# Performance work log

Hardware: AMD Instinct MI355X
Metric: run time of the kernel (lower is better)

Reference implementation:

```python
import jax, jax.numpy as jnp
import numpy as np

N = 30000   # fluid particles
E = 480000  # edges
F = 4       # fluidFeatures (in channels)
P = 8       # RBF basis size per dim (dims=[8], 1D)
LAYERS = [32, 64, 64, 2]


def hat_basis(x, n):
    # 'linear' RBF: hat functions on n evenly spaced centers in [-1, 1]
    centers = jnp.linspace(-1.0, 1.0, n, dtype=x.dtype)
    spacing = 2.0 / (n - 1)
    return jnp.maximum(0.0, 1.0 - jnp.abs(x[:, None] - centers[None, :]) / spacing)  # [E, n]


def rbf_conv(x, fi, fj, d, W, b, mask, n_nodes):
    # x: [N, Cin]; d: [E, 1] clamped; W: [P, Cin, Cout]; b: [Cout]
    phi = hat_basis(d[:, 0], W.shape[0])      # [E, P]
    xj = x[fj]                                 # gather source features [E, Cin]
    msg = jnp.zeros((xj.shape[0], W.shape[2]), dtype=x.dtype)
    for p in range(W.shape[0]):                # small fixed P=8 loop keeps memory O(E*Cout)
        msg = msg + phi[:, p, None] * (xj @ W[p])
    msg = jnp.where(mask[:, None], msg, 0.0)   # centerIgnore: drop self edges fi==fj
    out = jax.ops.segment_sum(msg, fi, num_segments=n_nodes)  # scatter-reduce to targets
    return out + b


def _xavier(key, shape_in, shape_out):
    lim = float(np.sqrt(6.0 / (shape_in + shape_out)))
    return jax.random.uniform(key, (shape_in, shape_out), jnp.float32, -lim, lim)


def setup_inputs() -> dict:
    key = jax.random.key(0)
    ks = jax.random.split(key, 16)
    fluidFeatures = jax.random.normal(ks[0], (N, F), jnp.float32)
    fi = jax.random.randint(ks[1], (E,), 0, N)
    fj = jax.random.randint(ks[2], (E,), 0, N)
    distances = jax.random.normal(ks[3], (E, 1), jnp.float32)
    # conv channels: 4->32, 64->64, 64->64, 64->2
    cio = [(F, 32), (2 * 32, 64), (64, 64), (64, 2)]
    inp = {"fluidFeatures": fluidFeatures, "fi": fi, "fj": fj, "distances": distances}
    for li, (ci, co) in enumerate(cio):
        inp[f"cW{li}"] = jax.random.normal(ks[4 + li], (P, ci, co), jnp.float32) * (1.0 / np.sqrt(P * ci))
        inp[f"cb{li}"] = jnp.zeros((co,), jnp.float32)
        inp[f"fW{li}"] = _xavier(ks[8 + li], ci, co)   # stored [in, out]
        inp[f"fb{li}"] = jnp.zeros((co,), jnp.float32)
    return inp


def reference(fluidFeatures, fi, fj, distances,
              cW0, cb0, fW0, fb0, cW1, cb1, fW1, fb1,
              cW2, cb2, fW2, fb2, cW3, cb3, fW3, fb3):
    n_nodes = fluidFeatures.shape[0]
    mask = fi != fj                     # centerIgnore (mask instead of filter: jit-safe)
    d = jnp.clip(distances, -1.0, 1.0)

    conv0 = rbf_conv(fluidFeatures, fi, fj, d, cW0, cb0, mask, n_nodes)  # [N, 32]
    lin0 = fluidFeatures @ fW0 + fb0                                      # [N, 32]
    ans = jnp.concatenate([lin0, conv0], axis=1)                          # [N, 64]

    # i = 1: features[0]=32 != features[1]=64 -> no residual
    ansc = jax.nn.relu(ans)
    ans = rbf_conv(ansc, fi, fj, d, cW1, cb1, mask, n_nodes) + (ansc @ fW1 + fb1)
    # i = 2: features[1]==features[2]==64 and shapes match -> residual
    ansc = jax.nn.relu(ans)
    ans = rbf_conv(ansc, fi, fj, d, cW2, cb2, mask, n_nodes) + (ansc @ fW2 + fb2) + ans
    # i = 3: 64 -> 2, no residual
    ansc = jax.nn.relu(ans)
    ans = rbf_conv(ansc, fi, fj, d, cW3, cb3, mask, n_nodes) + (ansc @ fW3 + fb3)

    return ans  # dim == 1 (dims=[8]) -> no /128
```

## Files before the change

### kernel.cpp

```cpp
#include <hip/hip_runtime.h>


#define CAP 48

typedef __attribute__((ext_vector_type(8))) short short8;
typedef __attribute__((ext_vector_type(4))) short short4v;
typedef __attribute__((ext_vector_type(4))) float f32x4;

__device__ __forceinline__ short bf16s(float f) {
  unsigned u = __float_as_uint(f);
  return (short)((u + 0x7FFF + ((u >> 16) & 1)) >> 16);
}
__device__ __forceinline__ float b2f(unsigned short s) {
  return __uint_as_float(((unsigned)s) << 16);
}
__device__ __forceinline__ unsigned pack2(float a, float b) {
  return (unsigned)(unsigned short)bf16s(a) | ((unsigned)(unsigned short)bf16s(b) << 16);
}
__device__ __forceinline__ float dec_w0(int v) {
  return __uint_as_float(0x3F800000u | (((unsigned)v & 0xFFFu) << 11)) - 1.0f;
}
__device__ __forceinline__ float dec_sf(int v) {
  return (float)(((unsigned)v >> 12) & 1u);
}

__global__ void fill_prep(const float* __restrict__ dist,
                          const int* __restrict__ fi, const int* __restrict__ fj,
                          int* __restrict__ cnt, int* __restrict__ jw, int nE,
                          const float* __restrict__ cW1, const float* __restrict__ fW1,
                          const float* __restrict__ cW2, const float* __restrict__ fW2,
                          short* __restrict__ wt1, short* __restrict__ wt2,
                          const float* __restrict__ X,
                          const float* __restrict__ cW0,
                          const float* __restrict__ fW0,
                          unsigned short* __restrict__ U0, int n,
                          int fillBlocks, int prepBlocks) {
  if ((int)blockIdx.x < fillBlocks) {
    int e = blockIdx.x * blockDim.x + threadIdx.x;
    if (e >= nE) return;
    int i = fi[e], j = fj[e];
    if (i == j) return;
    float d = fminf(1.0f, fmaxf(-1.0f, dist[e]));
    float u = (d + 1.0f) * 3.5f;
    int p = min((int)u, 6);
    float w0 = 1.0f - (u - (float)p);
    int wq = min((int)(w0 * 4096.0f + 0.5f), 4095);
    unsigned off = (unsigned)(j * 9 + p);
    int pos = atomicAdd(&cnt[i], 1);
    if (pos < CAP)
      jw[(size_t)i * CAP + pos] = (int)((off << 13) | 0x1000u | (unsigned)wq);
  } else if ((int)blockIdx.x < fillBlocks + prepBlocks) {
    int idx = ((int)blockIdx.x - fillBlocks) * blockDim.x + threadIdx.x;
    if (idx >= 2 * 576 * 64) return;
    int sel = idx / (576 * 64);
    int r = idx - sel * (576 * 64);
    int col = r >> 6, ch = r & 63;
    const float* cW = sel ? cW2 : cW1;
    const float* fW = sel ? fW2 : fW1;
    float v;
    if (col < 512) {
      int p = col >> 6, co = col & 63;
      v = cW[((size_t)p * 64 + ch) * 64 + co];
    } else {
      v = fW[(size_t)ch * 64 + (col - 512)];
    }
    (sel ? wt2 : wt1)[(size_t)col * 64 + ch] = bf16s(v);
  } else {
    int idx = ((int)blockIdx.x - fillBlocks - prepBlocks) * blockDim.x + threadIdx.x;
    if (idx >= n * 72) return;
    int i = idx / 72, g = idx - i * 72;
    float4 x = *(const float4*)(X + (size_t)i * 4);
    float xk[4] = {x.x, x.y, x.z, x.w};
    float s[4] = {0, 0, 0, 0};
    if (g < 64) {
      int p = g >> 3;
      int co = (g * 4) & 31;
      #pragma unroll
      for (int k = 0; k < 4; ++k) {
        const float* wr = cW0 + ((size_t)p * 4 + k) * 32 + co;
        #pragma unroll
        for (int c = 0; c < 4; ++c) s[c] = fmaf(xk[k], wr[c], s[c]);
      }
    } else {
      int co = (g - 64) * 4;
      #pragma unroll
      for (int k = 0; k < 4; ++k) {
        const float* wr = fW0 + (size_t)k * 32 + co;
        #pragma unroll
        for (int c = 0; c < 4; ++c) s[c] = fmaf(xk[k], wr[c], s[c]);
      }
    }
    uint2 pk = make_uint2(pack2(s[0], s[1]), pack2(s[2], s[3]));
    *(uint2*)(U0 + (size_t)i * 288 + g * 4) = pk;
  }
}

__device__ __forceinline__ void gemm_tail(const unsigned short* sXa, short* sUL,
                                          const short* __restrict__ WT,
                                          int w, int lane) {
  const int mrow = lane & 15;
  const int quad = lane >> 4;
  short8 b0 = *(const short8*)(sXa + mrow * 64 + quad * 8);
  short8 b1 = *(const short8*)(sXa + mrow * 64 + quad * 8 + 32);
  const short* A0 = WT + (size_t)(w * 16 + mrow) * 64 + quad * 8;
  const short* A1 = WT + (size_t)((w + 16) * 16 + mrow) * 64 + quad * 8;
  short8 a00 = *(const short8*)(A0);
  short8 a01 = *(const short8*)(A0 + 32);
  short8 a10 = *(const short8*)(A1);
  short8 a11 = *(const short8*)(A1 + 32);
  const bool has3 = (w < 4);
  short8 a20 = {0, 0, 0, 0, 0, 0, 0, 0};
  short8 a21 = {0, 0, 0, 0, 0, 0, 0, 0};
  if (has3) {
    const short* A2 = WT + (size_t)((w + 32) * 16 + mrow) * 64 + quad * 8;
    a20 = *(const short8*)(A2);
    a21 = *(const short8*)(A2 + 32);
  }
  __builtin_amdgcn_sched_barrier(0);
  f32x4 acc0 = {0, 0, 0, 0}, acc1 = {0, 0, 0, 0};
  acc0 = __builtin_amdgcn_mfma_f32_16x16x32_bf16(a00, b0, acc0, 0, 0, 0);
  acc0 = __builtin_amdgcn_mfma_f32_16x16x32_bf16(a01, b1, acc0, 0, 0, 0);
  acc1 = __builtin_amdgcn_mfma_f32_16x16x32_bf16(a10, b0, acc1, 0, 0, 0);
  acc1 = __builtin_amdgcn_mfma_f32_16x16x32_bf16(a11, b1, acc1, 0, 0, 0);
  short4v pk;
  #pragma unroll
  for (int r = 0; r < 4; ++r) pk[r] = bf16s(acc0[r]);
  *(short4v*)(sUL + mrow * 584 + w * 16 + quad * 4) = pk;
  #pragma unroll
  for (int r = 0; r < 4; ++r) pk[r] = bf16s(acc1[r]);
  *(short4v*)(sUL + mrow * 584 + (w + 16) * 16 + quad * 4) = pk;
  if (has3) {
    f32x4 acc2 = {0, 0, 0, 0};
    acc2 = __builtin_amdgcn_mfma_f32_16x16x32_bf16(a20, b0, acc2, 0, 0, 0);
    acc2 = __builtin_amdgcn_mfma_f32_16x16x32_bf16(a21, b1, acc2, 0, 0, 0);
    #pragma unroll
    for (int r = 0; r < 4; ++r) pk[r] = bf16s(acc2[r]);
    *(short4v*)(sUL + mrow * 584 + (w + 32) * 16 + quad * 4) = pk;
  }
}

__global__ __launch_bounds__(1024, 8) void layer0_gemm(
    const unsigned short* __restrict__ U0,
    const int* __restrict__ cnt, const int* __restrict__ jw,
    const float* __restrict__ cb0, const float* __restrict__ fb0,
    const short* __restrict__ WTul,
    unsigned short* __restrict__ UL, int n) {
  __shared__ __align__(16) unsigned short sXa[16 * 64];
  __shared__ __align__(16) short sUL[16 * 584];
  const int tid = threadIdx.x;
  const int w = tid >> 6;
  const int lane = tid & 63;
  const int grp = lane >> 5;
  const int gl = lane & 31;
  const unsigned gl4 = (unsigned)gl * 4u;
  const int nodeBase = blockIdx.x * 16;
  const int i = nodeBase + w;
  const bool valid = (i < n);
  const int ic = valid ? i : 0;
  const char* __restrict__ u0B = (const char*)U0;

  int rec = jw[(size_t)ic * CAP + (lane < CAP ? lane : 0)];
  const int m = valid ? min(cnt[ic], CAP) : 0;
  float accLo = 0.0f, accHi = 0.0f;
  unsigned rA[8], rB[8];
  float wA[8], wB[8];
#define L0_LOAD(R, WS, Q0)                                                  \
  _Pragma("unroll")                                                         \
  for (int k = 0; k < 8; ++k) {                                             \
    int vA = __builtin_amdgcn_readlane(rec, (Q0) + 2 * k);                  \
    int vB = __builtin_amdgcn_readlane(rec, (Q0) + 2 * k + 1);              \
    int v = grp ? vB : vA;                                                  \
    unsigned voff = (((unsigned)v >> 7) & 0xFFFFFFC0u) + gl4;               \
    R[k] = *(const unsigned*)(u0B + voff);                                  \
    float w0 = dec_w0(v);                                                   \
    WS[k] = (gl < 16) ? w0 : (dec_sf(v) - w0);                              \
  }
#define L0_FMA(R, WS)                                                       \
  _Pragma("unroll")                                                         \
  for (int k = 0; k < 8; ++k) {                                             \
    accLo = fmaf(WS[k], __uint_as_float(R[k] << 16), accLo);                \
    accHi = fmaf(WS[k], __uint_as_float(R[k] & 0xFFFF0000u), accHi);        \
  }
  if (m > 0) {
    L0_LOAD(rA, wA, 0);
    L0_LOAD(rB, wB, 16);
    __builtin_amdgcn_sched_barrier(0);
    L0_FMA(rA, wA);
    if (m > 16) {
      L0_FMA(rB, wB);
      for (int q0 = 32; q0 < m; q0 += 16) {
        L0_LOAD(rA, wA, q0);
        __builtin_amdgcn_sched_barrier(0);
        L0_FMA(rA, wA);
      }
    }
  }
#undef L0_LOAD
#undef L0_FMA
  accLo += __shfl_xor(accLo, 16, 64);
  accHi += __shfl_xor(accHi, 16, 64);
  accLo += __shfl_xor(accLo, 32, 64);
  accHi += __shfl_xor(accHi, 32, 64);
  if (lane < 16) {
    const int l = lane;
    float c0v = fmaxf(accLo + cb0[2 * l], 0.0f);
    float c1v = fmaxf(accHi + cb0[2 * l + 1], 0.0f);
    unsigned lr = ((const unsigned*)(U0 + (size_t)ic * 288 + 256))[l];
    float l0 = fmaxf(__uint_as_float(lr << 16) + fb0[2 * l], 0.0f);
    float l1 = fmaxf(__uint_as_float(lr & 0xFFFF0000u) + fb0[2 * l + 1], 0.0f);
    unsigned* row = (unsigned*)(sXa + w * 64);
    row[l] = pack2(l0, l1);
    row[16 + l] = pack2(c0v, c1v);
  }
  __syncthreads();

  gemm_tail(sXa, sUL, WTul, w, lane);
  __syncthreads();
  const int r = tid >> 6;
  const int c0 = tid & 63;
  if (nodeBase + r < n) {
    unsigned short* dst = UL + (size_t)(nodeBase + r) * 576;
    #pragma unroll
    for (int chunk = c0; chunk < 72; chunk += 64)
      *(short8*)(dst + chunk * 8) = *(const short8*)(sUL + r * 584 + chunk * 8);
  }
}

__global__ __launch_bounds__(1024, 8) void conv_gemm(
    const unsigned short* __restrict__ ULA,
    const int* __restrict__ cnt, const int* __restrict__ jw,
    const float* __restrict__ cb, const float* __restrict__ fb,
    const short* __restrict__ WTul2,
    float* __restrict__ outAns,
    unsigned short* __restrict__ ULB, int n) {
  __shared__ __align__(16) unsigned short sXa[16 * 64];
  __shared__ __align__(16) short sUL[16 * 584];
  const int tid = threadIdx.x;
  const int w = tid >> 6;
  const int lane = tid & 63;
  const int half = lane >> 5;
  const int pl = lane & 31;
  const unsigned lane4 = (unsigned)lane * 4u;
  const int nodeBase = blockIdx.x * 16;
  const int i = nodeBase + w;
  const bool valid = (i < n);
  const int ic = valid ? i : 0;
  const char* __restrict__ ulB = (const char*)ULA;

  int rec = jw[(size_t)ic * CAP + (lane < CAP ? lane : 0)];
  const int m = valid ? min(cnt[ic], CAP) : 0;
  const unsigned Lraw = ((const unsigned*)(ULA + (size_t)ic * 576 + 512))[pl];
  float accLo = 0.0f, accHi = 0.0f;
  unsigned rA[16], rB[16];
#define C1_LOAD(R, Q0)                                                     \
  _Pragma("unroll")                                                        \
  for (int k = 0; k < 16; ++k) {                                           \
    int v = __builtin_amdgcn_readlane(rec, (Q0) + k);                      \
    unsigned voff = (((unsigned)v >> 6) & 0xFFFFFF80u) + lane4;            \
    R[k] = *(const unsigned*)(ulB + voff);                                 \
  }
#define C1_FMA(R, Q0)                                                      \
  _Pragma("unroll")                                                        \
  for (int k = 0; k < 16; ++k) {                                           \
    int v = __builtin_amdgcn_readlane(rec, (Q0) + k);                      \
    float w0 = dec_w0(v);                                                  \
    float wv = half ? (dec_sf(v) - w0) : w0;                               \
    accLo = fmaf(wv, __uint_as_float(R[k] << 16), accLo);                  \
    accHi = fmaf(wv, __uint_as_float(R[k] & 0xFFFF0000u), accHi);          \
  }
  if (m > 0) {
    C1_LOAD(rA, 0);
    C1_LOAD(rB, 16);
    __builtin_amdgcn_sched_barrier(0);
    C1_FMA(rA, 0);
    if (m > 16) {
      C1_FMA(rB, 16);
      for (int q0 = 32; q0 < m; q0 += 16) {
        C1_LOAD(rA, q0);
        __builtin_amdgcn_sched_barrier(0);
        C1_FMA(rA, q0);
      }
    }
  }
#undef C1_LOAD
#undef C1_FMA
  accLo += __shfl_xor(accLo, 32, 64);
  accHi += __shfl_xor(accHi, 32, 64);
  if (half == 0) {
    unsigned* row = (unsigned*)(sXa + w * 64);
    if (valid) {
      const int c0i = 2 * pl, c1i = c0i + 1;
      float o0 = accLo + __uint_as_float(Lraw << 16) + cb[c0i] + fb[c0i];
      float o1 = accHi + __uint_as_float(Lraw & 0xFFFF0000u) + cb[c1i] + fb[c1i];
      *(float2*)(outAns + (size_t)i * 64 + c0i) = make_float2(o0, o1);
      row[pl] = pack2(fmaxf(o0, 0.0f), fmaxf(o1, 0.0f));
    } else {
      row[pl] = 0u;
    }
  }
  __syncthreads();

  gemm_tail(sXa, sUL, WTul2, w, lane);
  __syncthreads();
  const int r = tid >> 6;
  const int c0 = tid & 63;
  if (nodeBase + r < n) {
    unsigned short* dst = ULB + (size_t)(nodeBase + r) * 576;
    #pragma unroll
    for (int chunk = c0; chunk < 72; chunk += 64)
      *(short8*)(dst + chunk * 8) = *(const short8*)(sUL + r * 584 + chunk * 8);
  }
}

__global__ __launch_bounds__(256, 8) void conv2_kernel(
    const unsigned short* __restrict__ UL,
    const int* __restrict__ cnt, const int* __restrict__ jw,
    const float* __restrict__ cb, const float* __restrict__ fb,
    const float* __restrict__ resid,
    const float* __restrict__ cW3,
    float* __restrict__ T,
    unsigned short* __restrict__ outAnsc, int n) {
  const int lane = threadIdx.x & 63;
  const int half = lane >> 5;
  const int pl = lane & 31;
  const unsigned lane4 = (unsigned)lane * 4u;
  const int i = (blockIdx.x * blockDim.x + threadIdx.x) >> 6;
  if (i >= n) return;
  const char* __restrict__ ulB = (const char*)UL;
  int rec = jw[(size_t)i * CAP + (lane < CAP ? lane : 0)];
  const int m = min(cnt[i], CAP);
  const unsigned Lraw = ((const unsigned*)(UL + (size_t)i * 576 + 512))[pl];
  float2 rv = *(const float2*)(resid + (size_t)i * 64 + 2 * pl);
  float accLo = 0.0f, accHi = 0.0f;
  unsigned rA[16], rB[16];
#define C2_LOAD(R, Q0)                                                     \
  _Pragma("unroll")                                                        \
  for (int k = 0; k < 16; ++k) {                                           \
    int v = __builtin_amdgcn_readlane(rec, (Q0) + k);                      \
    unsigned voff = (((unsigned)v >> 6) & 0xFFFFFF80u) + lane4;            \
    R[k] = *(const unsigned*)(ulB + voff);                                 \
  }
#define C2_FMA(R, Q0)                                                      \
  _Pragma("unroll")                                                        \
  for (int k = 0; k < 16; ++k) {                                           \
    int v = __builtin_amdgcn_readlane(rec, (Q0) + k);                      \
    float w0 = dec_w0(v);                                                  \
    float wv = half ? (dec_sf(v) - w0) : w0;                               \
    accLo = fmaf(wv, __uint_as_float(R[k] << 16), accLo);                  \
    accHi = fmaf(wv, __uint_as_float(R[k] & 0xFFFF0000u), accHi);          \
  }
  if (m > 0) {
    C2_LOAD(rA, 0);
    C2_LOAD(rB, 16);
    __builtin_amdgcn_sched_barrier(0);
    C2_FMA(rA, 0);
    if (m > 16) {
      C2_FMA(rB, 16);
      for (int q0 = 32; q0 < m; q0 += 16) {
        C2_LOAD(rA, q0);
        __builtin_amdgcn_sched_barrier(0);
        C2_FMA(rA, q0);
      }
    }
  }
#undef C2_LOAD
#undef C2_FMA
  accLo += __shfl_xor(accLo, 32, 64);
  accHi += __shfl_xor(accHi, 32, 64);
  if (half == 0) {
    const int c0i = 2 * pl, c1i = c0i + 1;
    float o0 = accLo + __uint_as_float(Lraw << 16) + cb[c0i] + fb[c0i] + rv.x;
    float o1 = accHi + __uint_as_float(Lraw & 0xFFFF0000u) + cb[c1i] + fb[c1i] + rv.y;
    unsigned short xb0 = (unsigned short)bf16s(fmaxf(o0, 0.0f));
    unsigned short xb1 = (unsigned short)bf16s(fmaxf(o1, 0.0f));
    ((unsigned*)(outAnsc + (size_t)i * 64))[pl] = (unsigned)xb0 | ((unsigned)xb1 << 16);
    float x0 = b2f(xb0), x1 = b2f(xb1);
    float c[16];
    #pragma unroll
    for (int t = 0; t < 16; ++t) {
      const float* wrow = cW3 + ((size_t)(t >> 1) * 64) * 2 + (t & 1);
      c[t] = x0 * wrow[c0i * 2] + x1 * wrow[c1i * 2];
    }
    #pragma unroll
    for (int off = 16; off > 0; off >>= 1) {
      #pragma unroll
      for (int t = 0; t < 16; ++t) c[t] += __shfl_xor(c[t], off, 64);
    }
    if (pl == 0) {
      float* tr = T + (size_t)i * 18;
      #pragma unroll
      for (int t = 0; t < 16; ++t) tr[t] = c[t];
    }
  }
}

__global__ __launch_bounds__(256, 4) void layer3_kernel(
    const unsigned short* __restrict__ Xb,
    const float* __restrict__ T,
    const int* __restrict__ cnt, const int* __restrict__ jw,
    const float* __restrict__ cb3, const float* __restrict__ fb3,
    const float* __restrict__ fW3,
    float* __restrict__ out, int n) {
  const int lane = threadIdx.x & 63;
  const int i = (blockIdx.x * blockDim.x + threadIdx.x) >> 6;
  if (i >= n) return;
  const int m = min(cnt[i], CAP);
  float c0 = 0.0f, c1 = 0.0f;
  if (lane < m) {
    int v = jw[(size_t)i * CAP + lane];
    unsigned off = (unsigned)v >> 13;
    float w0 = dec_w0(v);
    float w1 = 1.0f - w0;
    const float* tb = T + (size_t)off * 2;
    float2 ta = *(const float2*)(tb);
    float2 tc = *(const float2*)(tb + 2);
    c0 = w0 * ta.x + w1 * tc.x;
    c1 = w0 * ta.y + w1 * tc.y;
  }
  float xi = b2f(Xb[(size_t)i * 64 + lane]);
  float2 fw = *(const float2*)(fW3 + lane * 2);
  c0 = fmaf(xi, fw.x, c0);
  c1 = fmaf(xi, fw.y, c1);
  #pragma unroll
  for (int off = 32; off > 0; off >>= 1) {
    c0 += __shfl_xor(c0, off, 64);
    c1 += __shfl_xor(c1, off, 64);
  }
  if (lane == 0) {
    out[(size_t)i * 2 + 0] = c0 + cb3[0] + fb3[0];
    out[(size_t)i * 2 + 1] = c1 + cb3[1] + fb3[1];
  }
}

extern "C" void kernel_launch(void* const* d_in, const int* in_sizes, int n_in,
                              void* d_out, int out_size, void* d_ws, size_t ws_size,
                              hipStream_t stream) {
  const float* X    = (const float*)d_in[0];
  const int*   fi   = (const int*)d_in[1];
  const int*   fj   = (const int*)d_in[2];
  const float* dist = (const float*)d_in[3];
  const float* cW0 = (const float*)d_in[4];  const float* cb0 = (const float*)d_in[5];
  const float* fW0 = (const float*)d_in[6];  const float* fb0 = (const float*)d_in[7];
  const float* cW1 = (const float*)d_in[8];  const float* cb1 = (const float*)d_in[9];
  const float* fW1 = (const float*)d_in[10]; const float* fb1 = (const float*)d_in[11];
  const float* cW2 = (const float*)d_in[12]; const float* cb2 = (const float*)d_in[13];
  const float* fW2 = (const float*)d_in[14]; const float* fb2 = (const float*)d_in[15];
  const float* cW3 = (const float*)d_in[16]; const float* cb3 = (const float*)d_in[17];
  const float* fW3 = (const float*)d_in[18]; const float* fb3 = (const float*)d_in[19];
  float* out = (float*)d_out;

  const int n  = in_sizes[0] / 4;
  const int nE = in_sizes[1];

  unsigned short* ULA   = (unsigned short*)d_ws;
  unsigned short* ULB   = ULA + (size_t)n * 576;
  unsigned short* U0    = ULB;
  float*          ans1  = (float*)(ULB + (size_t)n * 576);
  unsigned short* ansc2 = (unsigned short*)(ans1 + (size_t)n * 64);
  float* T     = (float*)(ansc2 + (size_t)n * 64);
  short* wtul1 = (short*)(T + (size_t)n * 18);
  short* wtul2 = wtul1 + 576 * 64;
  int*   jw    = (int*)(wtul2 + 576 * 64);
  int*   cnt   = jw + (size_t)n * CAP;

  hipMemsetAsync(jw, 0, ((size_t)n * CAP + n) * sizeof(int), stream);
  const int fillBlocks = (nE + 255) / 256;
  const int prepBlocks = (2 * 576 * 64 + 255) / 256;
  const int u0Blocks   = (n * 72 + 255) / 256;
  fill_prep<<<fillBlocks + prepBlocks + u0Blocks, 256, 0, stream>>>(
      dist, fi, fj, cnt, jw, nE, cW1, fW1, cW2, fW2, wtul1, wtul2,
      X, cW0, fW0, U0, n, fillBlocks, prepBlocks);

  layer0_gemm<<<(n + 15) / 16, 1024, 0, stream>>>(U0, cnt, jw, cb0, fb0,
                                                  wtul1, ULA, n);
  conv_gemm<<<(n + 15) / 16, 1024, 0, stream>>>(ULA, cnt, jw, cb1, fb1,
                                                wtul2, ans1, ULB, n);
  conv2_kernel<<<(n * 64 + 255) / 256, 256, 0, stream>>>(
      ULB, cnt, jw, cb2, fb2, ans1, cW3, T, ansc2, n);
  layer3_kernel<<<(n * 64 + 255) / 256, 256, 0, stream>>>(ansc2, T, cnt, jw,
                                                          cb3, fb3, fW3, out, n);
}
```

Before: 244.0 us.

## Load neighbor records via scalar loads and gather with inline-asm SGPR-based loads

Neighbor record rows and counts now come in through scalar s_load_dwordx4 instructions into SGPRs, replacing per-lane vector loads followed by readlane. The gathers use inline-asm global_load_dword with an SGPR base and VGPR offsets, issuing 16 or 32 loads before a single wait. The aim is to cut VALU and readlane overhead and raise memory-level parallelism in the gather loops. In exchange it adds heavy SGPR use, full vmcnt(0) waits with no overlap between batches, and inline asm that depends on the scalar-load alignment of rows.

```diff
diff --git a/kernel.cpp b/kernel.cpp
--- a/kernel.cpp
+++ b/kernel.cpp
@@ -6,6 +6,7 @@
 typedef __attribute__((ext_vector_type(8))) short short8;
 typedef __attribute__((ext_vector_type(4))) short short4v;
 typedef __attribute__((ext_vector_type(4))) float f32x4;
+typedef int v4i __attribute__((ext_vector_type(4)));
 
 __device__ __forceinline__ short bf16s(float f) {
   unsigned u = __float_as_uint(f);
@@ -23,6 +24,96 @@
 __device__ __forceinline__ float dec_sf(int v) {
   return (float)(((unsigned)v >> 12) & 1u);
 }
+__device__ __forceinline__ unsigned long long rfl64(unsigned long long x) {
+  unsigned lo = __builtin_amdgcn_readfirstlane((unsigned)x);
+  unsigned hi = __builtin_amdgcn_readfirstlane((unsigned)(x >> 32));
+  return ((unsigned long long)hi << 32) | (unsigned long long)lo;
+}
+
+#define LOAD_RECS32(JROW, CPTR, RC, MRAW)                                   \
+  {                                                                         \
+    v4i s0_, s1_, s2_, s3_, s4_, s5_, s6_, s7_;                             \
+    asm volatile(                                                           \
+        "s_load_dwordx4 %0, %9, 0x0\n\t"                                    \
+        "s_load_dwordx4 %1, %9, 0x10\n\t"                                   \
+        "s_load_dwordx4 %2, %9, 0x20\n\t"                                   \
+        "s_load_dwordx4 %3, %9, 0x30\n\t"                                   \
+        "s_load_dwordx4 %4, %9, 0x40\n\t"                                   \
+        "s_load_dwordx4 %5, %9, 0x50\n\t"                                   \
+        "s_load_dwordx4 %6, %9, 0x60\n\t"                                   \
+        "s_load_dwordx4 %7, %9, 0x70\n\t"                                   \
+        "s_load_dword %8, %10, 0x0\n\t"                                     \
+        "s_waitcnt lgkmcnt(0)"                                              \
+        : "=&s"(s0_), "=&s"(s1_), "=&s"(s2_), "=&s"(s3_),                   \
+          "=&s"(s4_), "=&s"(s5_), "=&s"(s6_), "=&s"(s7_), "=&s"(MRAW)       \
+        : "s"(JROW), "s"(CPTR)                                              \
+        : "memory");                                                        \
+    _Pragma("unroll") for (int z_ = 0; z_ < 4; ++z_) {                      \
+      RC[z_] = s0_[z_];      RC[4 + z_] = s1_[z_];                          \
+      RC[8 + z_] = s2_[z_];  RC[12 + z_] = s3_[z_];                         \
+      RC[16 + z_] = s4_[z_]; RC[20 + z_] = s5_[z_];                         \
+      RC[24 + z_] = s6_[z_]; RC[28 + z_] = s7_[z_];                         \
+    }                                                                       \
+  }
+
+#define LOAD_RECS16T(JROW, RT)                                              \
+  {                                                                         \
+    v4i t0_, t1_, t2_, t3_;                                                 \
+    asm volatile(                                                           \
+        "s_load_dwordx4 %0, %4, 0x80\n\t"                                   \
+        "s_load_dwordx4 %1, %4, 0x90\n\t"                                   \
+        "s_load_dwordx4 %2, %4, 0xA0\n\t"                                   \
+        "s_load_dwordx4 %3, %4, 0xB0\n\t"                                   \
+        "s_waitcnt lgkmcnt(0)"                                              \
+        : "=&s"(t0_), "=&s"(t1_), "=&s"(t2_), "=&s"(t3_)                    \
+        : "s"(JROW)                                                         \
+        : "memory");                                                        \
+    _Pragma("unroll") for (int z_ = 0; z_ < 4; ++z_) {                      \
+      RT[z_] = t0_[z_];      RT[4 + z_] = t1_[z_];                          \
+      RT[8 + z_] = t2_[z_];  RT[12 + z_] = t3_[z_];                         \
+    }                                                                       \
+  }
+
+#define GLDI(x) "global_load_dword %" #x ", %" #x ", %[bb]\n\t"
+
+#define GATHER8(R, BASE)                                                    \
+  asm volatile(                                                             \
+      GLDI(0) GLDI(1) GLDI(2) GLDI(3) GLDI(4) GLDI(5) GLDI(6) GLDI(7)       \
+      "s_waitcnt vmcnt(0)"                                                  \
+      : "+v"(R[0]), "+v"(R[1]), "+v"(R[2]), "+v"(R[3]), "+v"(R[4]),         \
+        "+v"(R[5]), "+v"(R[6]), "+v"(R[7])                                  \
+      : [bb] "s"(BASE)                                                      \
+      : "memory")
+
+#define GATHER16(R, BASE)                                                   \
+  asm volatile(                                                             \
+      GLDI(0) GLDI(1) GLDI(2) GLDI(3) GLDI(4) GLDI(5) GLDI(6) GLDI(7)       \
+      GLDI(8) GLDI(9) GLDI(10) GLDI(11) GLDI(12) GLDI(13) GLDI(14) GLDI(15) \
+      "s_waitcnt vmcnt(0)"                                                  \
+      : "+v"(R[0]), "+v"(R[1]), "+v"(R[2]), "+v"(R[3]), "+v"(R[4]),         \
+        "+v"(R[5]), "+v"(R[6]), "+v"(R[7]), "+v"(R[8]), "+v"(R[9]),         \
+        "+v"(R[10]), "+v"(R[11]), "+v"(R[12]), "+v"(R[13]), "+v"(R[14]),    \
+        "+v"(R[15])                                                         \
+      : [bb] "s"(BASE)                                                      \
+      : "memory")
+
+#define GATHER32(R, BASE)                                                   \
+  asm volatile(                                                             \
+      GLDI(0) GLDI(1) GLDI(2) GLDI(3) GLDI(4) GLDI(5) GLDI(6) GLDI(7)       \
+      GLDI(8) GLDI(9) GLDI(10) GLDI(11) GLDI(12) GLDI(13) GLDI(14) GLDI(15) \
+      GLDI(16) GLDI(17) GLDI(18) GLDI(19) GLDI(20) GLDI(21) GLDI(22)        \
+      GLDI(23) GLDI(24) GLDI(25) GLDI(26) GLDI(27) GLDI(28) GLDI(29)        \
+      GLDI(30) GLDI(31)                                                     \
+      "s_waitcnt vmcnt(0)"                                                  \
+      : "+v"(R[0]), "+v"(R[1]), "+v"(R[2]), "+v"(R[3]), "+v"(R[4]),         \
+        "+v"(R[5]), "+v"(R[6]), "+v"(R[7]), "+v"(R[8]), "+v"(R[9]),         \
+        "+v"(R[10]), "+v"(R[11]), "+v"(R[12]), "+v"(R[13]), "+v"(R[14]),    \
+        "+v"(R[15]), "+v"(R[16]), "+v"(R[17]), "+v"(R[18]), "+v"(R[19]),    \
+        "+v"(R[20]), "+v"(R[21]), "+v"(R[22]), "+v"(R[23]), "+v"(R[24]),    \
+        "+v"(R[25]), "+v"(R[26]), "+v"(R[27]), "+v"(R[28]), "+v"(R[29]),    \
+        "+v"(R[30]), "+v"(R[31])                                            \
+      : [bb] "s"(BASE)                                                      \
+      : "memory")
 
 __global__ void fill_prep(const float* __restrict__ dist,
                           const int* __restrict__ fi, const int* __restrict__ fj,
@@ -157,46 +248,56 @@
   const int i = nodeBase + w;
   const bool valid = (i < n);
   const int ic = valid ? i : 0;
-  const char* __restrict__ u0B = (const char*)U0;
-
-  int rec = jw[(size_t)ic * CAP + (lane < CAP ? lane : 0)];
-  const int m = valid ? min(cnt[ic], CAP) : 0;
+  const int* jrow = (const int*)rfl64((unsigned long long)(jw + (size_t)ic * CAP));
+  const int* cptr = (const int*)rfl64((unsigned long long)(cnt + ic));
+
+  int rc[32]; int mraw;
+  LOAD_RECS32(jrow, cptr, rc, mraw);
+  const int m = valid ? min(mraw, CAP) : 0;
   float accLo = 0.0f, accHi = 0.0f;
-  unsigned rA[8], rB[8];
-  float wA[8], wB[8];
-#define L0_LOAD(R, WS, Q0)                                                  \
-  _Pragma("unroll")                                                         \
-  for (int k = 0; k < 8; ++k) {                                             \
-    int vA = __builtin_amdgcn_readlane(rec, (Q0) + 2 * k);                  \
-    int vB = __builtin_amdgcn_readlane(rec, (Q0) + 2 * k + 1);              \
-    int v = grp ? vB : vA;                                                  \
-    unsigned voff = (((unsigned)v >> 7) & 0xFFFFFFC0u) + gl4;               \
-    R[k] = *(const unsigned*)(u0B + voff);                                  \
-    float w0 = dec_w0(v);                                                   \
-    WS[k] = (gl < 16) ? w0 : (dec_sf(v) - w0);                              \
-  }
-#define L0_FMA(R, WS)                                                       \
-  _Pragma("unroll")                                                         \
-  for (int k = 0; k < 8; ++k) {                                             \
-    accLo = fmaf(WS[k], __uint_as_float(R[k] << 16), accLo);                \
-    accHi = fmaf(WS[k], __uint_as_float(R[k] & 0xFFFF0000u), accHi);        \
+  unsigned r[16];
+  int vsel[16];
+#define L0_FMA1(K)                                                          \
+  {                                                                         \
+    float w0_ = dec_w0(vsel[K]);                                            \
+    float wgt_ = (gl < 16) ? w0_ : (dec_sf(vsel[K]) - w0_);                 \
+    accLo = fmaf(wgt_, __uint_as_float(r[K] << 16), accLo);                 \
+    accHi = fmaf(wgt_, __uint_as_float(r[K] & 0xFFFF0000u), accHi);         \
   }
   if (m > 0) {
-    L0_LOAD(rA, wA, 0);
-    L0_LOAD(rB, wB, 16);
-    __builtin_amdgcn_sched_barrier(0);
-    L0_FMA(rA, wA);
-    if (m > 16) {
-      L0_FMA(rB, wB);
-      for (int q0 = 32; q0 < m; q0 += 16) {
-        L0_LOAD(rA, wA, q0);
-        __builtin_amdgcn_sched_barrier(0);
-        L0_FMA(rA, wA);
-      }
-    }
-  }
-#undef L0_LOAD
-#undef L0_FMA
+    if (m <= 16) {
+      #pragma unroll
+      for (int k = 0; k < 8; ++k) {
+        vsel[k] = grp ? rc[2 * k + 1] : rc[2 * k];
+        r[k] = ((((unsigned)vsel[k]) >> 7) & 0xFFFFFFC0u) + gl4;
+      }
+      GATHER8(r, U0);
+      #pragma unroll
+      for (int k = 0; k < 8; ++k) L0_FMA1(k);
+    } else {
+      #pragma unroll
+      for (int k = 0; k < 16; ++k) {
+        vsel[k] = grp ? rc[2 * k + 1] : rc[2 * k];
+        r[k] = ((((unsigned)vsel[k]) >> 7) & 0xFFFFFFC0u) + gl4;
+      }
+      GATHER16(r, U0);
+      #pragma unroll
+      for (int k = 0; k < 16; ++k) L0_FMA1(k);
+      if (m > 32) {
+        int rt[16];
+        LOAD_RECS16T(jrow, rt);
+        #pragma unroll
+        for (int k = 0; k < 8; ++k) {
+          vsel[k] = grp ? rt[2 * k + 1] : rt[2 * k];
+          r[k] = ((((unsigned)vsel[k]) >> 7) & 0xFFFFFFC0u) + gl4;
+        }
+        GATHER8(r, U0);
+        #pragma unroll
+        for (int k = 0; k < 8; ++k) L0_FMA1(k);
+      }
+    }
+  }
+#undef L0_FMA1
   accLo += __shfl_xor(accLo, 16, 64);
   accHi += __shfl_xor(accHi, 16, 64);
   accLo += __shfl_xor(accLo, 32, 64);
@@ -216,13 +317,13 @@
 
   gemm_tail(sXa, sUL, WTul, w, lane);
   __syncthreads();
-  const int r = tid >> 6;
+  const int r2 = tid >> 6;
   const int c0 = tid & 63;
-  if (nodeBase + r < n) {
-    unsigned short* dst = UL + (size_t)(nodeBase + r) * 576;
+  if (nodeBase + r2 < n) {
+    unsigned short* dst = UL + (size_t)(nodeBase + r2) * 576;
     #pragma unroll
     for (int chunk = c0; chunk < 72; chunk += 64)
-      *(short8*)(dst + chunk * 8) = *(const short8*)(sUL + r * 584 + chunk * 8);
+      *(short8*)(dst + chunk * 8) = *(const short8*)(sUL + r2 * 584 + chunk * 8);
   }
 }
 
@@ -245,45 +346,47 @@
   const int i = nodeBase + w;
   const bool valid = (i < n);
   const int ic = valid ? i : 0;
-  const char* __restrict__ ulB = (const char*)ULA;
-
-  int rec = jw[(size_t)ic * CAP + (lane < CAP ? lane : 0)];
-  const int m = valid ? min(cnt[ic], CAP) : 0;
+  const int* jrow = (const int*)rfl64((unsigned long long)(jw + (size_t)ic * CAP));
+  const int* cptr = (const int*)rfl64((unsigned long long)(cnt + ic));
+
+  int rc[32]; int mraw;
+  LOAD_RECS32(jrow, cptr, rc, mraw);
+  const int m = valid ? min(mraw, CAP) : 0;
   const unsigned Lraw = ((const unsigned*)(ULA + (size_t)ic * 576 + 512))[pl];
   float accLo = 0.0f, accHi = 0.0f;
-  unsigned rA[16], rB[16];
-#define C1_LOAD(R, Q0)                                                     \
-  _Pragma("unroll")                                                        \
-  for (int k = 0; k < 16; ++k) {                                           \
-    int v = __builtin_amdgcn_readlane(rec, (Q0) + k);                      \
-    unsigned voff = (((unsigned)v >> 6) & 0xFFFFFF80u) + lane4;            \
-    R[k] = *(const unsigned*)(ulB + voff);                                 \
-  }
-#define C1_FMA(R, Q0)                                                      \
-  _Pragma("unroll")                                                        \
-  for (int k = 0; k < 16; ++k) {                                           \
-    int v = __builtin_amdgcn_readlane(rec, (Q0) + k);                      \
-    float w0 = dec_w0(v);                                                  \
-    float wv = half ? (dec_sf(v) - w0) : w0;                               \
-    accLo = fmaf(wv, __uint_as_float(R[k] << 16), accLo);                  \
-    accHi = fmaf(wv, __uint_as_float(R[k] & 0xFFFF0000u), accHi);          \
+  unsigned r[32];
+#define CV_OFF(V) (((((unsigned)(V)) >> 6) & 0xFFFFFF80u) + lane4)
+#define CV_FMA(V, RD)                                                       \
+  {                                                                         \
+    float w0_ = dec_w0(V);                                                  \
+    float wv_ = half ? (dec_sf(V) - w0_) : w0_;                             \
+    accLo = fmaf(wv_, __uint_as_float((RD) << 16), accLo);                  \
+    accHi = fmaf(wv_, __uint_as_float((RD) & 0xFFFF0000u), accHi);          \
   }
   if (m > 0) {
-    C1_LOAD(rA, 0);
-    C1_LOAD(rB, 16);
-    __builtin_amdgcn_sched_barrier(0);
-    C1_FMA(rA, 0);
-    if (m > 16) {
-      C1_FMA(rB, 16);
-      for (int q0 = 32; q0 < m; q0 += 16) {
-        C1_LOAD(rA, q0);
-        __builtin_amdgcn_sched_barrier(0);
-        C1_FMA(rA, q0);
-      }
-    }
-  }
-#undef C1_LOAD
-#undef C1_FMA
+    if (m <= 16) {
+      #pragma unroll
+      for (int k = 0; k < 16; ++k) r[k] = CV_OFF(rc[k]);
+      GATHER16(r, ULA);
+      #pragma unroll
+      for (int k = 0; k < 16; ++k) CV_FMA(rc[k], r[k]);
+    } else {
+      #pragma unroll
+      for (int k = 0; k < 32; ++k) r[k] = CV_OFF(rc[k]);
+      GATHER32(r, ULA);
+      #pragma unroll
+      for (int k = 0; k < 32; ++k) CV_FMA(rc[k], r[k]);
+      if (m > 32) {
+        int rt[16];
+        LOAD_RECS16T(jrow, rt);
+        #pragma unroll
+        for (int k = 0; k < 16; ++k) r[k] = CV_OFF(rt[k]);
+        GATHER16(r, ULA);
+        #pragma unroll
+        for (int k = 0; k < 16; ++k) CV_FMA(rt[k], r[k]);
+      }
+    }
+  }
   accLo += __shfl_xor(accLo, 32, 64);
   accHi += __shfl_xor(accHi, 32, 64);
   if (half == 0) {
@@ -302,13 +405,13 @@
 
   gemm_tail(sXa, sUL, WTul2, w, lane);
   __syncthreads();
-  const int r = tid >> 6;
+  const int r2 = tid >> 6;
   const int c0 = tid & 63;
-  if (nodeBase + r < n) {
-    unsigned short* dst = ULB + (size_t)(nodeBase + r) * 576;
+  if (nodeBase + r2 < n) {
+    unsigned short* dst = ULB + (size_t)(nodeBase + r2) * 576;
     #pragma unroll
     for (int chunk = c0; chunk < 72; chunk += 64)
-      *(short8*)(dst + chunk * 8) = *(const short8*)(sUL + r * 584 + chunk * 8);
+      *(short8*)(dst + chunk * 8) = *(const short8*)(sUL + r2 * 584 + chunk * 8);
   }
 }
 
@@ -326,45 +429,39 @@
   const unsigned lane4 = (unsigned)lane * 4u;
   const int i = (blockIdx.x * blockDim.x + threadIdx.x) >> 6;
   if (i >= n) return;
-  const char* __restrict__ ulB = (const char*)UL;
-  int rec = jw[(size_t)i * CAP + (lane < CAP ? lane : 0)];
-  const int m = min(cnt[i], CAP);
+  const int* jrow = (const int*)rfl64((unsigned long long)(jw + (size_t)i * CAP));
+  const int* cptr = (const int*)rfl64((unsigned long long)(cnt + i));
+  int rc[32]; int mraw;
+  LOAD_RECS32(jrow, cptr, rc, mraw);
+  const int m = min(mraw, CAP);
   const unsigned Lraw = ((const unsigned*)(UL + (size_t)i * 576 + 512))[pl];
   float2 rv = *(const float2*)(resid + (size_t)i * 64 + 2 * pl);
   float accLo = 0.0f, accHi = 0.0f;
-  unsigned rA[16], rB[16];
-#define C2_LOAD(R, Q0)                                                     \
-  _Pragma("unroll")                                                        \
-  for (int k = 0; k < 16; ++k) {                                           \
-    int v = __builtin_amdgcn_readlane(rec, (Q0) + k);                      \
-    unsigned voff = (((unsigned)v >> 6) & 0xFFFFFF80u) + lane4;            \
-    R[k] = *(const unsigned*)(ulB + voff);                                 \
-  }
-#define C2_FMA(R, Q0)                                                      \
-  _Pragma("unroll")                                                        \
-  for (int k = 0; k < 16; ++k) {                                           \
-    int v = __builtin_amdgcn_readlane(rec, (Q0) + k);                      \
-    float w0 = dec_w0(v);                                                  \
-    float wv = half ? (dec_sf(v) - w0) : w0;                               \
-    accLo = fmaf(wv, __uint_as_float(R[k] << 16), accLo);                  \
-    accHi = fmaf(wv, __uint_as_float(R[k] & 0xFFFF0000u), accHi);          \
-  }
+  unsigned r[32];
   if (m > 0) {
-    C2_LOAD(rA, 0);
-    C2_LOAD(rB, 16);
-    __builtin_amdgcn_sched_barrier(0);
-    C2_FMA(rA, 0);
-    if (m > 16) {
-      C2_FMA(rB, 16);
-      for (int q0 = 32; q0 < m; q0 += 16) {
-        C2_LOAD(rA, q0);
-        __builtin_amdgcn_sched_barrier(0);
-        C2_FMA(rA, q0);
-      }
-    }
-  }
-#undef C2_LOAD
-#undef C2_FMA
+    if (m <= 16) {
+      #pragma unroll
+      for (int k = 0; k < 16; ++k) r[k] = CV_OFF(rc[k]);
+      GATHER16(r, UL);
+      #pragma unroll
+      for (int k = 0; k < 16; ++k) CV_FMA(rc[k], r[k]);
+    } else {
+      #pragma unroll
+      for (int k = 0; k < 32; ++k) r[k] = CV_OFF(rc[k]);
+      GATHER32(r, UL);
+      #pragma unroll
+      for (int k = 0; k < 32; ++k) CV_FMA(rc[k], r[k]);
+      if (m > 32) {
+        int rt[16];
+        LOAD_RECS16T(jrow, rt);
+        #pragma unroll
+        for (int k = 0; k < 16; ++k) r[k] = CV_OFF(rt[k]);
+        GATHER16(r, UL);
+        #pragma unroll
+        for (int k = 0; k < 16; ++k) CV_FMA(rt[k], r[k]);
+      }
+    }
+  }
   accLo += __shfl_xor(accLo, 32, 64);
   accHi += __shfl_xor(accHi, 32, 64);
   if (half == 0) {
```

Result: slower. 283.8 us (+16.3%).
